# Optimization experiments

Hardware: AMD Instinct MI355X
Metric: run time of the kernel (lower is better)

Reference implementation:

```python
import jax, jax.numpy as jnp
import numpy as np

MARGIN = 1.5  # init kwarg
N, M, K = 8192, 128, 16


def setup_inputs() -> dict:
    key = jax.random.key(0)
    k1, k2 = jax.random.split(key)
    feature = jax.random.normal(k1, (N, M), dtype=jnp.float32)
    # binary multi-labels in {0,1}; k=16 channels makes an all-zero row vanishingly rare
    label = jax.random.randint(k2, (N, K), 0, 2, dtype=jnp.int32)
    return {"feature": feature, "label": label}


def reference(feature, label):
    n, m = feature.shape
    # --- pair weights: IoU of positive label sets ------------------------
    # original: ((l_i == l_j) & (l_i > 0.5)).sum() / ((l_i > 0.5) | (l_j > 0.5)).sum()
    # for binary labels this is |pos_i & pos_j| / |pos_i | pos_j|
    pos = (label > 0).astype(jnp.float32)          # [n,k]
    npos = pos.sum(axis=1)                          # [n]
    inter = pos @ pos.T                             # [n,n] intersection counts
    union = npos[:, None] + npos[None, :] - inter   # [n,n] union counts
    weight = inter / union                          # 0/0 -> nan, same as torch
    weight = jnp.where(weight == 0, -1.0, weight)   # weight[weight==0] = -1
    # --- pairwise Euclidean distance via Gram trick ----------------------
    sq = jnp.sum(feature * feature, axis=1)         # [n]
    d2 = sq[:, None] + sq[None, :] - 2.0 * (feature @ feature.T)
    d2 = jnp.maximum(d2, 0.0)
    pos_d2 = d2 > 0
    dist = jnp.where(pos_d2, jnp.sqrt(jnp.where(pos_d2, d2, 1.0)), 0.0)
    dist = dist / np.sqrt(m).astype(np.float32)
    # --- margin-clipped weighted loss ------------------------------------
    loss = weight * jnp.minimum(dist, MARGIN)
    return loss.mean()
```

## Files before the change

### kernel.cpp

```cpp
#include <hip/hip_runtime.h>

#define NROW 8192
#define MDIM 128
#define KLAB 16
#define NSLAB 64
#define NTILE (NSLAB*(NSLAB+1)/2)
#define MARGINP  16.970562748477139f
#define MARGINP2 288.0f

typedef __attribute__((ext_vector_type(8))) short  s16x8;
typedef __attribute__((ext_vector_type(4))) float  f32x4;

#if __has_builtin(__builtin_amdgcn_sqrtf)
#define FSQRT(x) __builtin_amdgcn_sqrtf(x)
#else
#define FSQRT(x) sqrtf(x)
#endif
#if __has_builtin(__builtin_amdgcn_rcpf)
#define FRCP(x) __builtin_amdgcn_rcpf(x)
#else
#define FRCP(x) (1.0f / (x))
#endif
#if __has_builtin(__builtin_amdgcn_fmed3f)
#define FCLAMP(x) __builtin_amdgcn_fmed3f((x), 0.0f, MARGINP2)
#else
#define FCLAMP(x) fminf(fmaxf((x), 0.0f), MARGINP2)
#endif

__device__ __forceinline__ unsigned short f2bf(float x) {
  unsigned u = __float_as_uint(x);
  return (unsigned short)((u + 0x7FFFu + ((u >> 16) & 1u)) >> 16);
}

__global__ void prep_kernel(const float* __restrict__ feat, const int* __restrict__ label,
                            unsigned short* __restrict__ fbf, float* __restrict__ sq,
                            int* __restrict__ maskA) {
  int wv = threadIdx.x >> 6, lane = threadIdx.x & 63;
  int sub = lane >> 4, l16 = lane & 15;
  int row = blockIdx.x * 16 + wv * 4 + sub;
  const float* rp = feat + (size_t)row * MDIM + l16 * 8;
  float4 va = *reinterpret_cast<const float4*>(rp);
  float4 vb = *reinterpret_cast<const float4*>(rp + 4);
  s16x8 st;
  st[0]=(short)f2bf(va.x); st[1]=(short)f2bf(va.y); st[2]=(short)f2bf(va.z); st[3]=(short)f2bf(va.w);
  st[4]=(short)f2bf(vb.x); st[5]=(short)f2bf(vb.y); st[6]=(short)f2bf(vb.z); st[7]=(short)f2bf(vb.w);
  *reinterpret_cast<s16x8*>(fbf + (size_t)row * MDIM + l16 * 8) = st;
  float s = va.x*va.x + va.y*va.y + va.z*va.z + va.w*va.w
          + vb.x*vb.x + vb.y*vb.y + vb.z*vb.z + vb.w*vb.w;
  #pragma unroll
  for (int off = 8; off >= 1; off >>= 1) s += __shfl_xor(s, off);
  int lab = label[((size_t)blockIdx.x * 16 + wv * 4) * KLAB + lane];
  unsigned long long bal = __ballot(lab > 0);
  if (l16 == 0) {
    sq[row]    = s;
    maskA[row] = (int)(unsigned)((bal >> (sub * 16)) & 0xFFFFull);
  }
}

__global__ __launch_bounds__(512, 2) void pair_main(
    const unsigned short* __restrict__ fbf, const float* __restrict__ sq,
    const int* __restrict__ maskA, float* __restrict__ part) {
  __shared__ char smem[65536];
  __shared__ float bsum[8];

  int bi = 0, rem = blockIdx.x;
  while (rem >= NSLAB - bi) { rem -= NSLAB - bi; bi++; }
  int bj = bi + rem;
  bool diag = (bi == bj);

  int wv = threadIdx.x >> 6, lane = threadIdx.x & 63;
  int l15 = lane & 15, lg = lane >> 4;
  int wr = wv >> 1, wc = wv & 1;

  {
    const char* gA = (const char*)(fbf + (size_t)bi * 128 * MDIM);
    const char* gB = (const char*)(fbf + (size_t)bj * 128 * MDIM);
    int sub = lane >> 4, c = lane & 15;
    #pragma unroll
    for (int t = 0; t < 4; t++) {
      int lr = wv * 16 + t * 4 + sub;
      s16x8 va = *reinterpret_cast<const s16x8*>(gA + lr * 256 + c * 16);
      s16x8 vb = *reinterpret_cast<const s16x8*>(gB + lr * 256 + c * 16);
      int wck = c ^ (lr & 7);
      *reinterpret_cast<s16x8*>(smem + lr * 256 + wck * 16) = va;
      *reinterpret_cast<s16x8*>(smem + 32768 + lr * 256 + wck * 16) = vb;
    }
  }

  float sqi[2][4]; int mi[2][4];
  #pragma unroll
  for (int fi = 0; fi < 2; fi++)
    #pragma unroll
    for (int r = 0; r < 4; r++) {
      int ir = bi * 128 + wr * 32 + fi * 16 + lg * 4 + r;
      sqi[fi][r] = sq[ir]; mi[fi][r] = maskA[ir];
    }
  float sqj[4]; int mj[4];
  #pragma unroll
  for (int fj = 0; fj < 4; fj++) {
    int jr = bj * 128 + wc * 64 + fj * 16 + l15;
    sqj[fj] = sq[jr]; mj[fj] = maskA[jr];
  }

  __syncthreads();

  s16x8 af[2][4];
  #pragma unroll
  for (int fi = 0; fi < 2; fi++)
    #pragma unroll
    for (int ks = 0; ks < 4; ks++) {
      int lr = wr * 32 + fi * 16 + l15;
      int rc = (ks * 4 + lg) ^ (lr & 7);
      af[fi][ks] = *reinterpret_cast<const s16x8*>(smem + lr * 256 + rc * 16);
    }

  float sum = 0.0f;

  #pragma unroll
  for (int fj = 0; fj < 4; fj++) {
    s16x8 B[4];
    #pragma unroll
    for (int ks = 0; ks < 4; ks++) {
      int lr = wc * 64 + fj * 16 + l15;
      int rc = (ks * 4 + lg) ^ (lr & 7);
      B[ks] = *reinterpret_cast<const s16x8*>(smem + 32768 + lr * 256 + rc * 16);
    }

    f32x4 acc[2];
    acc[0] = (f32x4){0.f,0.f,0.f,0.f}; acc[1] = (f32x4){0.f,0.f,0.f,0.f};
    #pragma unroll
    for (int ks = 0; ks < 4; ks++)
      #pragma unroll
      for (int fi = 0; fi < 2; fi++)
        acc[fi] = __builtin_amdgcn_mfma_f32_16x16x32_bf16(af[fi][ks], B[ks], acc[fi], 0, 0, 0);

    #pragma unroll
    for (int fi = 0; fi < 2; fi++)
      #pragma unroll
      for (int r = 0; r < 4; r++) {
        float g  = acc[fi][r];
        float d2 = fmaf(-2.0f, g, sqi[fi][r] + sqj[fj]);
        float t  = FSQRT(FCLAMP(d2));
        int inter = __popc(mi[fi][r] & mj[fj]);
        int uni   = __popc(mi[fi][r] | mj[fj]);
        float w = (float)inter * FRCP((float)uni);
        w = (inter == 0) ? -1.0f : w;
        if (diag) {
          int il = wr * 32 + fi * 16 + lg * 4 + r;
          int jl = wc * 64 + fj * 16 + l15;
          w *= (jl > il) ? 2.0f : ((jl == il) ? 1.0f : 0.0f);
        }
        sum = fmaf(w, t, sum);
      }
  }

  #pragma unroll
  for (int off = 32; off >= 1; off >>= 1) sum += __shfl_xor(sum, off);
  if (lane == 0) bsum[wv] = sum;
  __syncthreads();
  if (threadIdx.x == 0) {
    float s = 0.f;
    #pragma unroll
    for (int w = 0; w < 8; w++) s += bsum[w];
    part[blockIdx.x] = diag ? s : 2.0f * s;
  }
}

__global__ void reduce_kernel(const float* __restrict__ part, float* __restrict__ out) {
  int tid = threadIdx.x;
  double s = 0.0;
  for (int i = tid; i < NTILE; i += 256) s += (double)part[i];
  #pragma unroll
  for (int off = 32; off >= 1; off >>= 1) s += __shfl_xor(s, off);
  __shared__ double wsum[4];
  int wv = tid >> 6, lane = tid & 63;
  if (lane == 0) wsum[wv] = s;
  __syncthreads();
  if (tid == 0) {
    double t = wsum[0] + wsum[1] + wsum[2] + wsum[3];
    out[0] = (float)(t * (1.0 / (11.313708498984760 * 67108864.0)));
  }
}

extern "C" void kernel_launch(void* const* d_in, const int* in_sizes, int n_in,
                              void* d_out, int out_size, void* d_ws, size_t ws_size,
                              hipStream_t stream) {
  const float* feat  = (const float*)d_in[0];
  const int*   label = (const int*)d_in[1];
  char* ws = (char*)d_ws;
  float* part           = (float*)ws;
  float* sq             = (float*)(ws + 8448);
  int*   maskA          = (int*)(ws + 8448 + 32768);
  unsigned short* fbf   = (unsigned short*)(ws + 8448 + 65536);
  float* out = (float*)d_out;

  prep_kernel<<<NROW / 16, 256, 0, stream>>>(feat, label, fbf, sq, maskA);
  pair_main<<<NTILE, 512, 0, stream>>>(fbf, sq, maskA, part);
  reduce_kernel<<<1, 256, 0, stream>>>(part, out);
}
```

Before: 40.11 us.

## Split pair tiles into half-blocks, load A fragments directly, swizzle block order

Each 128x128 tile is now split into two 64x128 halves handled by 256-thread blocks, which doubles the grid and halves shared memory per block so more blocks fit per CU. The A operand fragments are read straight from global memory into registers instead of going through LDS, and only B is staged in shared memory. A block-index swizzle groups neighbouring tiles across XCD-interleaved blocks to improve cache locality. The cost is that each B slab is now loaded twice, by the two halves, and there are twice as many partial sums to reduce.

```diff
diff --git a/kernel.cpp b/kernel.cpp
--- a/kernel.cpp
+++ b/kernel.cpp
@@ -4,7 +4,8 @@
 #define MDIM 128
 #define KLAB 16
 #define NSLAB 64
-#define NTILE (NSLAB*(NSLAB+1)/2)
+#define NSUPER (NSLAB*(NSLAB+1)/2)
+#define NBLK (NSUPER*2)
 #define MARGINP  16.970562748477139f
 #define MARGINP2 288.0f
 
@@ -57,13 +58,17 @@
   }
 }
 
-__global__ __launch_bounds__(512, 2) void pair_main(
+__global__ __launch_bounds__(256, 4) void pair_main(
     const unsigned short* __restrict__ fbf, const float* __restrict__ sq,
     const int* __restrict__ maskA, float* __restrict__ part) {
-  __shared__ char smem[65536];
-  __shared__ float bsum[8];
-
-  int bi = 0, rem = blockIdx.x;
+  __shared__ char smem[32768];
+  __shared__ float bsum[4];
+
+  int orig = blockIdx.x;
+  int swz = (orig & 7) * (NBLK / 8) + (orig >> 3);
+  int sid = swz >> 1, half = swz & 1;
+
+  int bi = 0, rem = sid;
   while (rem >= NSLAB - bi) { rem -= NSLAB - bi; bi++; }
   int bj = bi + rem;
   bool diag = (bi == bj);
@@ -72,27 +77,23 @@
   int l15 = lane & 15, lg = lane >> 4;
   int wr = wv >> 1, wc = wv & 1;
 
-  {
-    const char* gA = (const char*)(fbf + (size_t)bi * 128 * MDIM);
-    const char* gB = (const char*)(fbf + (size_t)bj * 128 * MDIM);
-    int sub = lane >> 4, c = lane & 15;
-    #pragma unroll
-    for (int t = 0; t < 4; t++) {
-      int lr = wv * 16 + t * 4 + sub;
-      s16x8 va = *reinterpret_cast<const s16x8*>(gA + lr * 256 + c * 16);
-      s16x8 vb = *reinterpret_cast<const s16x8*>(gB + lr * 256 + c * 16);
-      int wck = c ^ (lr & 7);
-      *reinterpret_cast<s16x8*>(smem + lr * 256 + wck * 16) = va;
-      *reinterpret_cast<s16x8*>(smem + 32768 + lr * 256 + wck * 16) = vb;
-    }
-  }
+  const char* fb = (const char*)fbf;
+  int arow = bi * 128 + half * 64 + wr * 32;
+
+  s16x8 af[2][4];
+  #pragma unroll
+  for (int fi = 0; fi < 2; fi++)
+    #pragma unroll
+    for (int ks = 0; ks < 4; ks++)
+      af[fi][ks] = *reinterpret_cast<const s16x8*>(
+          fb + (size_t)(arow + fi * 16 + l15) * 256 + ks * 64 + lg * 16);
 
   float sqi[2][4]; int mi[2][4];
   #pragma unroll
   for (int fi = 0; fi < 2; fi++)
     #pragma unroll
     for (int r = 0; r < 4; r++) {
-      int ir = bi * 128 + wr * 32 + fi * 16 + lg * 4 + r;
+      int ir = arow + fi * 16 + lg * 4 + r;
       sqi[fi][r] = sq[ir]; mi[fi][r] = maskA[ir];
     }
   float sqj[4]; int mj[4];
@@ -102,17 +103,18 @@
     sqj[fj] = sq[jr]; mj[fj] = maskA[jr];
   }
 
+  {
+    const char* gB = fb + (size_t)bj * 128 * 256;
+    #pragma unroll
+    for (int k = 0; k < 8; k++) {
+      int f = threadIdx.x + 256 * k;
+      int row = f >> 4, c = f & 15;
+      s16x8 v = *reinterpret_cast<const s16x8*>(gB + row * 256 + c * 16);
+      int wck = c ^ (row & 7);
+      *reinterpret_cast<s16x8*>(smem + row * 256 + wck * 16) = v;
+    }
+  }
   __syncthreads();
-
-  s16x8 af[2][4];
-  #pragma unroll
-  for (int fi = 0; fi < 2; fi++)
-    #pragma unroll
-    for (int ks = 0; ks < 4; ks++) {
-      int lr = wr * 32 + fi * 16 + l15;
-      int rc = (ks * 4 + lg) ^ (lr & 7);
-      af[fi][ks] = *reinterpret_cast<const s16x8*>(smem + lr * 256 + rc * 16);
-    }
 
   float sum = 0.0f;
 
@@ -123,7 +125,7 @@
     for (int ks = 0; ks < 4; ks++) {
       int lr = wc * 64 + fj * 16 + l15;
       int rc = (ks * 4 + lg) ^ (lr & 7);
-      B[ks] = *reinterpret_cast<const s16x8*>(smem + 32768 + lr * 256 + rc * 16);
+      B[ks] = *reinterpret_cast<const s16x8*>(smem + lr * 256 + rc * 16);
     }
 
     f32x4 acc[2];
@@ -146,7 +148,7 @@
         float w = (float)inter * FRCP((float)uni);
         w = (inter == 0) ? -1.0f : w;
         if (diag) {
-          int il = wr * 32 + fi * 16 + lg * 4 + r;
+          int il = half * 64 + wr * 32 + fi * 16 + lg * 4 + r;
           int jl = wc * 64 + fj * 16 + l15;
           w *= (jl > il) ? 2.0f : ((jl == il) ? 1.0f : 0.0f);
         }
@@ -159,17 +161,15 @@
   if (lane == 0) bsum[wv] = sum;
   __syncthreads();
   if (threadIdx.x == 0) {
-    float s = 0.f;
-    #pragma unroll
-    for (int w = 0; w < 8; w++) s += bsum[w];
-    part[blockIdx.x] = diag ? s : 2.0f * s;
+    float s = bsum[0] + bsum[1] + bsum[2] + bsum[3];
+    part[orig] = diag ? s : 2.0f * s;
   }
 }
 
 __global__ void reduce_kernel(const float* __restrict__ part, float* __restrict__ out) {
   int tid = threadIdx.x;
   double s = 0.0;
-  for (int i = tid; i < NTILE; i += 256) s += (double)part[i];
+  for (int i = tid; i < NBLK; i += 256) s += (double)part[i];
   #pragma unroll
   for (int off = 32; off >= 1; off >>= 1) s += __shfl_xor(s, off);
   __shared__ double wsum[4];
@@ -189,12 +189,12 @@
   const int*   label = (const int*)d_in[1];
   char* ws = (char*)d_ws;
   float* part           = (float*)ws;
-  float* sq             = (float*)(ws + 8448);
-  int*   maskA          = (int*)(ws + 8448 + 32768);
-  unsigned short* fbf   = (unsigned short*)(ws + 8448 + 65536);
+  float* sq             = (float*)(ws + 16896);
+  int*   maskA          = (int*)(ws + 16896 + 32768);
+  unsigned short* fbf   = (unsigned short*)(ws + 16896 + 65536);
   float* out = (float*)d_out;
 
   prep_kernel<<<NROW / 16, 256, 0, stream>>>(feat, label, fbf, sq, maskA);
-  pair_main<<<NTILE, 512, 0, stream>>>(fbf, sq, maskA, part);
+  pair_main<<<NBLK, 256, 0, stream>>>(fbf, sq, maskA, part);
   reduce_kernel<<<1, 256, 0, stream>>>(part, out);
 }
```

Result: slower. 44.71 us (+11.5%).

## Compute label intersections with fp8 MFMA and load A fragments directly from global

Applied to the files above, without the earlier changes.

Label positives are now stored as fp8 ones (0x38) per channel. The pairwise intersection counts come from an fp8 16x16x32 MFMA instead of per-element popcounts. The union is derived from precomputed per-row positive counts packed with the squared norms into a float2. A fragments are read straight from global memory into registers instead of being staged through LDS, which halves shared memory use and could allow more resident blocks. The trade-off is one extra MFMA per fragment pair, uncoalesced global reads for the A operand, and an exact-count dependence on fp8 ones summed in fp32.

```diff
diff --git a/kernel.cpp b/kernel.cpp
--- a/kernel.cpp
+++ b/kernel.cpp
@@ -5,7 +5,6 @@
 #define KLAB 16
 #define NSLAB 64
 #define NTILE (NSLAB*(NSLAB+1)/2)
-#define MARGINP  16.970562748477139f
 #define MARGINP2 288.0f
 
 typedef __attribute__((ext_vector_type(8))) short  s16x8;
@@ -33,8 +32,8 @@
 }
 
 __global__ void prep_kernel(const float* __restrict__ feat, const int* __restrict__ label,
-                            unsigned short* __restrict__ fbf, float* __restrict__ sq,
-                            int* __restrict__ maskA) {
+                            unsigned short* __restrict__ fbf, float2* __restrict__ sqnp,
+                            unsigned char* __restrict__ posf8) {
   int wv = threadIdx.x >> 6, lane = threadIdx.x & 63;
   int sub = lane >> 4, l16 = lane & 15;
   int row = blockIdx.x * 16 + wv * 4 + sub;
@@ -50,17 +49,19 @@
   #pragma unroll
   for (int off = 8; off >= 1; off >>= 1) s += __shfl_xor(s, off);
   int lab = label[((size_t)blockIdx.x * 16 + wv * 4) * KLAB + lane];
-  unsigned long long bal = __ballot(lab > 0);
+  bool on = lab > 0;
+  unsigned long long bal = __ballot(on);
+  posf8[(size_t)row * KLAB + l16] = on ? 0x38 : 0x00;
   if (l16 == 0) {
-    sq[row]    = s;
-    maskA[row] = (int)(unsigned)((bal >> (sub * 16)) & 0xFFFFull);
+    unsigned m = (unsigned)((bal >> (sub * 16)) & 0xFFFFull);
+    sqnp[row] = make_float2(s, (float)__popc(m));
   }
 }
 
 __global__ __launch_bounds__(512, 2) void pair_main(
-    const unsigned short* __restrict__ fbf, const float* __restrict__ sq,
-    const int* __restrict__ maskA, float* __restrict__ part) {
-  __shared__ char smem[65536];
+    const unsigned short* __restrict__ fbf, const float2* __restrict__ sqnp,
+    const unsigned char* __restrict__ posf8, float* __restrict__ part) {
+  __shared__ char smem[32768];
   __shared__ float bsum[8];
 
   int bi = 0, rem = blockIdx.x;
@@ -71,80 +72,101 @@
   int wv = threadIdx.x >> 6, lane = threadIdx.x & 63;
   int l15 = lane & 15, lg = lane >> 4;
   int wr = wv >> 1, wc = wv & 1;
+  const char* fb = (const char*)fbf;
+  int arow = bi * 128 + wr * 32;
+
+  s16x8 af[2][4];
+  #pragma unroll
+  for (int fi = 0; fi < 2; fi++)
+    #pragma unroll
+    for (int ks = 0; ks < 4; ks++)
+      af[fi][ks] = *reinterpret_cast<const s16x8*>(
+          fb + (size_t)(arow + fi * 16 + l15) * 256 + ks * 64 + lg * 16);
+  long long alab[2];
+  #pragma unroll
+  for (int fi = 0; fi < 2; fi++) {
+    int row = arow + fi * 16 + l15;
+    alab[fi] = (lg < 2) ? *reinterpret_cast<const long long*>(posf8 + (size_t)row * KLAB + lg * 8)
+                        : 0LL;
+  }
+
+  float sqi[2][4], nif[2][4];
+  #pragma unroll
+  for (int fi = 0; fi < 2; fi++)
+    #pragma unroll
+    for (int r = 0; r < 4; r++) {
+      float2 v = sqnp[arow + fi * 16 + lg * 4 + r];
+      sqi[fi][r] = v.x; nif[fi][r] = v.y;
+    }
+  float sqj[4], njf[4];
+  #pragma unroll
+  for (int fj = 0; fj < 4; fj++) {
+    float2 v = sqnp[bj * 128 + wc * 64 + fj * 16 + l15];
+    sqj[fj] = v.x; njf[fj] = v.y;
+  }
 
   {
-    const char* gA = (const char*)(fbf + (size_t)bi * 128 * MDIM);
-    const char* gB = (const char*)(fbf + (size_t)bj * 128 * MDIM);
-    int sub = lane >> 4, c = lane & 15;
-    #pragma unroll
-    for (int t = 0; t < 4; t++) {
-      int lr = wv * 16 + t * 4 + sub;
-      s16x8 va = *reinterpret_cast<const s16x8*>(gA + lr * 256 + c * 16);
-      s16x8 vb = *reinterpret_cast<const s16x8*>(gB + lr * 256 + c * 16);
-      int wck = c ^ (lr & 7);
-      *reinterpret_cast<s16x8*>(smem + lr * 256 + wck * 16) = va;
-      *reinterpret_cast<s16x8*>(smem + 32768 + lr * 256 + wck * 16) = vb;
-    }
-  }
-
-  float sqi[2][4]; int mi[2][4];
-  #pragma unroll
-  for (int fi = 0; fi < 2; fi++)
-    #pragma unroll
-    for (int r = 0; r < 4; r++) {
-      int ir = bi * 128 + wr * 32 + fi * 16 + lg * 4 + r;
-      sqi[fi][r] = sq[ir]; mi[fi][r] = maskA[ir];
-    }
-  float sqj[4]; int mj[4];
+    const char* gB = fb + (size_t)bj * 128 * 256;
+    int tid = threadIdx.x;
+    #pragma unroll
+    for (int k = 0; k < 4; k++) {
+      int f = tid + 512 * k;
+      int row = f >> 4, c = f & 15;
+      s16x8 v = *reinterpret_cast<const s16x8*>(gB + row * 256 + c * 16);
+      int wck = c ^ (row & 7);
+      *reinterpret_cast<s16x8*>(smem + row * 256 + wck * 16) = v;
+    }
+  }
+  __syncthreads();
+
+  float sum = 0.0f;
+
   #pragma unroll
   for (int fj = 0; fj < 4; fj++) {
-    int jr = bj * 128 + wc * 64 + fj * 16 + l15;
-    sqj[fj] = sq[jr]; mj[fj] = maskA[jr];
-  }
-
-  __syncthreads();
-
-  s16x8 af[2][4];
-  #pragma unroll
-  for (int fi = 0; fi < 2; fi++)
+    int jrow = wc * 64 + fj * 16 + l15;
+    s16x8 B[4];
     #pragma unroll
     for (int ks = 0; ks < 4; ks++) {
-      int lr = wr * 32 + fi * 16 + l15;
-      int rc = (ks * 4 + lg) ^ (lr & 7);
-      af[fi][ks] = *reinterpret_cast<const s16x8*>(smem + lr * 256 + rc * 16);
-    }
-
-  float sum = 0.0f;
-
-  #pragma unroll
-  for (int fj = 0; fj < 4; fj++) {
-    s16x8 B[4];
-    #pragma unroll
-    for (int ks = 0; ks < 4; ks++) {
-      int lr = wc * 64 + fj * 16 + l15;
-      int rc = (ks * 4 + lg) ^ (lr & 7);
-      B[ks] = *reinterpret_cast<const s16x8*>(smem + 32768 + lr * 256 + rc * 16);
-    }
-
-    f32x4 acc[2];
-    acc[0] = (f32x4){0.f,0.f,0.f,0.f}; acc[1] = (f32x4){0.f,0.f,0.f,0.f};
+      int rc = (ks * 4 + lg) ^ (jrow & 7);
+      B[ks] = *reinterpret_cast<const s16x8*>(smem + jrow * 256 + rc * 16);
+    }
+    long long blab = (lg < 2) ? *reinterpret_cast<const long long*>(
+                                    posf8 + (size_t)(bj * 128 + jrow) * KLAB + lg * 8)
+                              : 0LL;
+
+    f32x4 acc[2], icc[2];
+    #pragma unroll
+    for (int fi = 0; fi < 2; fi++) {
+      acc[fi] = (f32x4){0.f,0.f,0.f,0.f};
+      icc[fi] = (f32x4){0.f,0.f,0.f,0.f};
+    }
     #pragma unroll
     for (int ks = 0; ks < 4; ks++)
       #pragma unroll
       for (int fi = 0; fi < 2; fi++)
         acc[fi] = __builtin_amdgcn_mfma_f32_16x16x32_bf16(af[fi][ks], B[ks], acc[fi], 0, 0, 0);
-
+    #pragma unroll
+    for (int fi = 0; fi < 2; fi++)
+      icc[fi] = __builtin_amdgcn_mfma_f32_16x16x32_fp8_fp8(alab[fi], blab, icc[fi], 0, 0, 0);
+
+    float sqs[2][4], usum[2][4];
     #pragma unroll
     for (int fi = 0; fi < 2; fi++)
       #pragma unroll
       for (int r = 0; r < 4; r++) {
-        float g  = acc[fi][r];
-        float d2 = fmaf(-2.0f, g, sqi[fi][r] + sqj[fj]);
+        sqs[fi][r]  = sqi[fi][r] + sqj[fj];
+        usum[fi][r] = nif[fi][r] + njf[fj];
+      }
+
+    #pragma unroll
+    for (int fi = 0; fi < 2; fi++)
+      #pragma unroll
+      for (int r = 0; r < 4; r++) {
+        float inter = icc[fi][r];
+        float d2 = fmaf(-2.0f, acc[fi][r], sqs[fi][r]);
         float t  = FSQRT(FCLAMP(d2));
-        int inter = __popc(mi[fi][r] & mj[fj]);
-        int uni   = __popc(mi[fi][r] | mj[fj]);
-        float w = (float)inter * FRCP((float)uni);
-        w = (inter == 0) ? -1.0f : w;
+        float w  = inter * FRCP(usum[fi][r] - inter);
+        w = (inter == 0.0f) ? -1.0f : w;
         if (diag) {
           int il = wr * 32 + fi * 16 + lg * 4 + r;
           int jl = wc * 64 + fj * 16 + l15;
@@ -188,13 +210,13 @@
   const float* feat  = (const float*)d_in[0];
   const int*   label = (const int*)d_in[1];
   char* ws = (char*)d_ws;
-  float* part           = (float*)ws;
-  float* sq             = (float*)(ws + 8448);
-  int*   maskA          = (int*)(ws + 8448 + 32768);
-  unsigned short* fbf   = (unsigned short*)(ws + 8448 + 65536);
+  float*          part  = (float*)ws;
+  float2*         sqnp  = (float2*)(ws + 16384);
+  unsigned char*  posf8 = (unsigned char*)(ws + 16384 + 65536);
+  unsigned short* fbf   = (unsigned short*)(ws + 16384 + 65536 + 131072);
   float* out = (float*)d_out;
 
-  prep_kernel<<<NROW / 16, 256, 0, stream>>>(feat, label, fbf, sq, maskA);
-  pair_main<<<NTILE, 512, 0, stream>>>(fbf, sq, maskA, part);
+  prep_kernel<<<NROW / 16, 256, 0, stream>>>(feat, label, fbf, sqnp, posf8);
+  pair_main<<<NTILE, 512, 0, stream>>>(fbf, sqnp, posf8, part);
   reduce_kernel<<<1, 256, 0, stream>>>(part, out);
 }
```

After: 70.05 us. 74.6% more time.

## Fuse final reduction into pair kernel via atomic ticket and pack sq/mask

Applied to the files above, without the earlier changes.

Removes the separate reduce kernel launch by having the last finishing pair_main block, detected with an atomic ticket counter, perform the final double-precision reduction. Squared norms and label masks are packed into one float2 array so each row needs a single load. The union count is now derived from precomputed per-row popcounts, saving one popcount per pair. The exchange is a memset launch for the ticket plus a threadfence and atomic per block.

```diff
diff --git a/kernel.cpp b/kernel.cpp
--- a/kernel.cpp
+++ b/kernel.cpp
@@ -5,7 +5,6 @@
 #define KLAB 16
 #define NSLAB 64
 #define NTILE (NSLAB*(NSLAB+1)/2)
-#define MARGINP  16.970562748477139f
 #define MARGINP2 288.0f
 
 typedef __attribute__((ext_vector_type(8))) short  s16x8;
@@ -33,8 +32,7 @@
 }
 
 __global__ void prep_kernel(const float* __restrict__ feat, const int* __restrict__ label,
-                            unsigned short* __restrict__ fbf, float* __restrict__ sq,
-                            int* __restrict__ maskA) {
+                            unsigned short* __restrict__ fbf, float2* __restrict__ sqm) {
   int wv = threadIdx.x >> 6, lane = threadIdx.x & 63;
   int sub = lane >> 4, l16 = lane & 15;
   int row = blockIdx.x * 16 + wv * 4 + sub;
@@ -52,16 +50,18 @@
   int lab = label[((size_t)blockIdx.x * 16 + wv * 4) * KLAB + lane];
   unsigned long long bal = __ballot(lab > 0);
   if (l16 == 0) {
-    sq[row]    = s;
-    maskA[row] = (int)(unsigned)((bal >> (sub * 16)) & 0xFFFFull);
+    int m = (int)(unsigned)((bal >> (sub * 16)) & 0xFFFFull);
+    sqm[row] = make_float2(s, __int_as_float(m));
   }
 }
 
 __global__ __launch_bounds__(512, 2) void pair_main(
-    const unsigned short* __restrict__ fbf, const float* __restrict__ sq,
-    const int* __restrict__ maskA, float* __restrict__ part) {
+    const unsigned short* __restrict__ fbf, const float2* __restrict__ sqm,
+    float* __restrict__ part, int* __restrict__ ticket, float* __restrict__ out) {
   __shared__ char smem[65536];
   __shared__ float bsum[8];
+  __shared__ int lastFlag;
+  __shared__ double wsumD[8];
 
   int bi = 0, rem = blockIdx.x;
   while (rem >= NSLAB - bi) { rem -= NSLAB - bi; bi++; }
@@ -87,19 +87,23 @@
     }
   }
 
-  float sqi[2][4]; int mi[2][4];
+  float sqi[2][4], nif[2][4]; int mi[2][4];
   #pragma unroll
   for (int fi = 0; fi < 2; fi++)
     #pragma unroll
     for (int r = 0; r < 4; r++) {
-      int ir = bi * 128 + wr * 32 + fi * 16 + lg * 4 + r;
-      sqi[fi][r] = sq[ir]; mi[fi][r] = maskA[ir];
-    }
-  float sqj[4]; int mj[4];
+      float2 v = sqm[bi * 128 + wr * 32 + fi * 16 + lg * 4 + r];
+      sqi[fi][r] = v.x;
+      int m = __float_as_int(v.y);
+      mi[fi][r] = m; nif[fi][r] = (float)__popc(m);
+    }
+  float sqj[4], njf[4]; int mj[4];
   #pragma unroll
   for (int fj = 0; fj < 4; fj++) {
-    int jr = bj * 128 + wc * 64 + fj * 16 + l15;
-    sqj[fj] = sq[jr]; mj[fj] = maskA[jr];
+    float2 v = sqm[bj * 128 + wc * 64 + fj * 16 + l15];
+    sqj[fj] = v.x;
+    int m = __float_as_int(v.y);
+    mj[fj] = m; njf[fj] = (float)__popc(m);
   }
 
   __syncthreads();
@@ -134,17 +138,25 @@
       for (int fi = 0; fi < 2; fi++)
         acc[fi] = __builtin_amdgcn_mfma_f32_16x16x32_bf16(af[fi][ks], B[ks], acc[fi], 0, 0, 0);
 
+    float sqs[2][4], nsf[2][4];
     #pragma unroll
     for (int fi = 0; fi < 2; fi++)
       #pragma unroll
       for (int r = 0; r < 4; r++) {
-        float g  = acc[fi][r];
-        float d2 = fmaf(-2.0f, g, sqi[fi][r] + sqj[fj]);
+        sqs[fi][r] = sqi[fi][r] + sqj[fj];
+        nsf[fi][r] = nif[fi][r] + njf[fj];
+      }
+
+    #pragma unroll
+    for (int fi = 0; fi < 2; fi++)
+      #pragma unroll
+      for (int r = 0; r < 4; r++) {
+        float d2 = fmaf(-2.0f, acc[fi][r], sqs[fi][r]);
         float t  = FSQRT(FCLAMP(d2));
-        int inter = __popc(mi[fi][r] & mj[fj]);
-        int uni   = __popc(mi[fi][r] | mj[fj]);
-        float w = (float)inter * FRCP((float)uni);
-        w = (inter == 0) ? -1.0f : w;
+        int   ic = __popc(mi[fi][r] & mj[fj]);
+        float icf = (float)ic;
+        float w  = icf * FRCP(nsf[fi][r] - icf);
+        w = (ic == 0) ? -1.0f : w;
         if (diag) {
           int il = wr * 32 + fi * 16 + lg * 4 + r;
           int jl = wc * 64 + fj * 16 + l15;
@@ -163,22 +175,26 @@
     #pragma unroll
     for (int w = 0; w < 8; w++) s += bsum[w];
     part[blockIdx.x] = diag ? s : 2.0f * s;
-  }
-}
-
-__global__ void reduce_kernel(const float* __restrict__ part, float* __restrict__ out) {
-  int tid = threadIdx.x;
-  double s = 0.0;
-  for (int i = tid; i < NTILE; i += 256) s += (double)part[i];
-  #pragma unroll
-  for (int off = 32; off >= 1; off >>= 1) s += __shfl_xor(s, off);
-  __shared__ double wsum[4];
-  int wv = tid >> 6, lane = tid & 63;
-  if (lane == 0) wsum[wv] = s;
+    __threadfence();
+    lastFlag = (atomicAdd(ticket, 1) == NTILE - 1);
+  }
   __syncthreads();
-  if (tid == 0) {
-    double t = wsum[0] + wsum[1] + wsum[2] + wsum[3];
-    out[0] = (float)(t * (1.0 / (11.313708498984760 * 67108864.0)));
+
+  if (lastFlag) {
+    __threadfence();
+    int tid = threadIdx.x;
+    double s = 0.0;
+    for (int i = tid; i < NTILE; i += 512) s += (double)part[i];
+    #pragma unroll
+    for (int off = 32; off >= 1; off >>= 1) s += __shfl_xor(s, off);
+    if (lane == 0) wsumD[wv] = s;
+    __syncthreads();
+    if (tid == 0) {
+      double t = 0.0;
+      #pragma unroll
+      for (int w = 0; w < 8; w++) t += wsumD[w];
+      out[0] = (float)(t * (1.0 / (11.313708498984760 * 67108864.0)));
+    }
   }
 }
 
@@ -188,13 +204,13 @@
   const float* feat  = (const float*)d_in[0];
   const int*   label = (const int*)d_in[1];
   char* ws = (char*)d_ws;
-  float* part           = (float*)ws;
-  float* sq             = (float*)(ws + 8448);
-  int*   maskA          = (int*)(ws + 8448 + 32768);
-  unsigned short* fbf   = (unsigned short*)(ws + 8448 + 65536);
+  int*            ticket = (int*)ws;
+  float*          part   = (float*)(ws + 256);
+  float2*         sqm    = (float2*)(ws + 16384);
+  unsigned short* fbf    = (unsigned short*)(ws + 16384 + 65536);
   float* out = (float*)d_out;
 
-  prep_kernel<<<NROW / 16, 256, 0, stream>>>(feat, label, fbf, sq, maskA);
-  pair_main<<<NTILE, 512, 0, stream>>>(fbf, sq, maskA, part);
-  reduce_kernel<<<1, 256, 0, stream>>>(part, out);
-}
+  (void)hipMemsetAsync(ticket, 0, sizeof(int), stream);
+  prep_kernel<<<NROW / 16, 256, 0, stream>>>(feat, label, fbf, sqm);
+  pair_main<<<NTILE, 512, 0, stream>>>(fbf, sqm, part, ticket, out);
+}
```

New measurement: 97.38 us. +142.8%, slower.
